# Optimization experiments

Hardware: AMD Instinct MI355X
Metric: run time of the kernel (lower is better)

The kernel has to match this reference:

```python
import jax, jax.numpy as jnp
import numpy as np

B, N, T = 16, 512, 12
IN, HID, HH, EMB, K, OUT = 2, 32, 32, 16, 2, 12


def setup_inputs() -> dict:
    key = jax.random.key(0)
    ks = jax.random.split(key, 32)
    def r(i, sh, s=1.0):
        return jax.random.normal(ks[i], sh, dtype=jnp.float32) * s
    return {
        "times": jnp.arange(T, dtype=jnp.float32),
        "coeff_a": r(0, (B, N, T - 1, IN)),
        "coeff_b": r(1, (B, N, T - 1, IN), 0.1),
        "coeff_c2": r(2, (B, N, T - 1, IN), 0.05),
        "coeff_d3": r(3, (B, N, T - 1, IN), 0.02),
        "Wh": r(4, (IN, HID), 0.3), "bh": r(5, (HID,), 0.01),
        "Wz": r(6, (IN, HID), 0.3), "bz": r(7, (HID,), 0.01),
        "fWin": r(8, (HID, HH), 0.15), "fbin": r(9, (HH,), 0.01),
        "fWmid": r(10, (HH, HH), 0.15), "fbmid": r(11, (HH,), 0.01),
        "fWout": r(12, (HH, HID * IN), 0.15), "fbout": r(13, (HID * IN,), 0.01),
        "gWin": r(14, (HID, HH), 0.15), "gbin": r(15, (HH,), 0.01),
        "gE": r(16, (N, EMB), 0.3),
        "gWpool": r(17, (EMB, K, HH, HH), 0.1),
        "gbpool": r(18, (EMB, HH), 0.1),
        "gWout": r(19, (HH, HID * HID), 0.05), "gbout": r(20, (HID * HID,), 0.01),
        "convW": r(21, (OUT, HID), 0.1), "convb": r(22, (OUT,), 0.01),
    }


def _forward(times, coeff_a, coeff_b, coeff_c2, coeff_d3, Wh, bh, Wz, bz,
             fWin, fbin, fWmid, fbmid, fWout, fbout,
             gWin, gbin, gE, gWpool, gbpool, gWout, gbout, convW, convb):
    maxlen = coeff_b.shape[2] - 1  # T - 2

    def dXdt(t):
        # NaturalCubicSpline.derivative: b + (two_c + three_d * frac) * frac
        idx = jnp.clip(jnp.sum(t > times) - 1, 0, maxlen)
        frac = t - times[idx]
        b = jnp.take(coeff_b, idx, axis=2)    # (B,N,IN)
        c2 = jnp.take(coeff_c2, idx, axis=2)
        d3 = jnp.take(coeff_d3, idx, axis=2)
        return b + (c2 + d3 * frac) * frac

    # adaptive graph conv supports + per-node weights (depend on params only)
    A = jax.nn.softmax(jax.nn.relu(gE @ gE.T), axis=1)   # (N,N)
    sup = [jnp.eye(N, dtype=A.dtype), A]
    for _ in range(2, K):
        sup.append(2.0 * A @ sup[-1] - sup[-2])
    supports = jnp.stack(sup, axis=0)                     # (K,N,N)
    aw = jnp.einsum('nd,dkio->nkio', gE, gWpool)          # (N,K,HH,HH)
    ab = gE @ gbpool                                      # (N,HH)

    def func_f(h):  # (B,N,HID) -> (B,N,HID,IN)
        x = jax.nn.relu(h @ fWin + fbin)
        x = jax.nn.relu(x @ fWmid + fbmid)
        return jnp.tanh((x @ fWout + fbout).reshape(*x.shape[:-1], HID, IN))

    def func_g(z):  # (B,N,HID) -> (B,N,HID,HID)
        x = jax.nn.relu(z @ gWin + gbin)                  # (B,N,HH)
        xg = jnp.einsum('knm,bmc->bnkc', supports, x)     # (B,N,K,HH)
        x = jnp.einsum('bnki,nkio->bno', xg, aw) + ab     # (B,N,HH)
        return jnp.tanh((x @ gWout + gbout).reshape(*x.shape[:-1], HID, HID))

    def vfield(t, h, z):
        dX = dXdt(t)                                      # (B,N,IN)
        vf = func_f(h)                                    # (B,N,HID,IN)
        vg = func_g(z)                                    # (B,N,HID,HID)
        fg = jnp.einsum('bnho,bnoi->bnhi', vg, vf)        # g(z) @ f(h)
        dh = jnp.einsum('bnhi,bni->bnh', vf, dX)
        dz = jnp.einsum('bnhi,bni->bnh', fg, dX)
        return dh, dz

    x0 = coeff_a[:, :, 0, :]          # spline.evaluate(times[0]) = a[...,0,:]
    h0 = x0 @ Wh + bh
    z0 = x0 @ Wz + bz

    def step(carry, tt):
        # torchdiffeq 'rk4' = RK4 with 3/8 rule (rk4_alt_step_func)
        h, z = carry
        t0, t1 = tt
        dt = t1 - t0
        third = dt / 3.0
        k1h, k1z = vfield(t0, h, z)
        k2h, k2z = vfield(t0 + third, h + third * k1h, z + third * k1z)
        k3h, k3z = vfield(t0 + 2.0 * third,
                          h + dt * (k2h - k1h / 3.0), z + dt * (k2z - k1z / 3.0))
        k4h, k4z = vfield(t1,
                          h + dt * (k1h - k2h + k3h), z + dt * (k1z - k2z + k3z))
        h = h + dt * 0.125 * (k1h + 3.0 * (k2h + k3h) + k4h)
        z = z + dt * 0.125 * (k1z + 3.0 * (k2z + k3z) + k4z)
        return (h, z), None

    (hT, zT), _ = jax.lax.scan(step, (h0, z0), (times[:-1], times[1:]))

    # end_conv: Conv2d(1, OUT, kernel=(1, HID)) on z_T (B,1,N,HID) -> (B,OUT,N,1)
    out = jnp.einsum('bnh,oh->bon', zT, convW) + convb[None, :, None]
    out = out.reshape(B, 1, OUT, N).transpose(0, 1, 3, 2)  # (B,1,N,OUT)
    return out


def reference(times, coeff_a, coeff_b, coeff_c2, coeff_d3, Wh, bh, Wz, bz,
              fWin, fbin, fWmid, fbmid, fWout, fbout,
              gWin, gbin, gE, gWpool, gbpool, gWout, gbout, convW, convb):
    return _forward(times, coeff_a, coeff_b, coeff_c2, coeff_d3, Wh, bh, Wz, bz,
                    fWin, fbin, fWmid, fbmid, fWout, fbout,
                    gWin, gbin, gE, gWpool, gbpool, gWout, gbout, convW, convb)
```

## Files before the change

### kernel.cpp

```cpp
#include <hip/hip_runtime.h>
#include <math.h>

#define NPTS 8192
#define NPS  (NPTS*32)

typedef __attribute__((ext_vector_type(8))) short bf16x8;
typedef __attribute__((ext_vector_type(4))) float f32x4;

__device__ __forceinline__ float tanh_fast(float x) {
  float e = __expf(2.0f*x);
  return 1.0f - 2.0f*__builtin_amdgcn_rcpf(e + 1.0f);
}
__device__ __forceinline__ unsigned short bf16h(float x) {
  unsigned u = __float_as_uint(x);
  return (unsigned short)((u + 0x7FFFu + ((u>>16)&1u)) >> 16);
}
__device__ __forceinline__ float bf16f(unsigned short h) {
  return __uint_as_float(((unsigned)h)<<16);
}
__device__ __forceinline__ bf16x8 pack_hi(const float* base) {
  bf16x8 H;
  #pragma unroll
  for (int jj = 0; jj < 4; ++jj) {
    float2 q = *(const float2*)(base + 2*jj);
// ... 76 lines not shown

__global__ void kPackGW(const float* __restrict__ gWout, short* __restrict__ GpkH,
                        short* __restrict__ GpkL) {
  int idx = blockIdx.x*256 + threadIdx.x;
  int j = idx & 7, l = (idx>>3)&63, tl = idx>>9;
  int col = tl*16 + (l&15);
  int k = ((l>>4)&3)*8 + j;
  float v = gWout[k*1024 + col];
  unsigned short hb = bf16h(v);
  GpkH[idx] = (short)hb;
  GpkL[idx] = (short)bf16h(v - bf16f(hb));
}

__global__ void kPackW(const float* __restrict__ fWin, const float* __restrict__ fWmid,
                       const float* __restrict__ fWout, const float* __restrict__ gWin,
                       short* __restrict__ WpkH, short* __restrict__ WpkL) {
  int idx = blockIdx.x*256 + threadIdx.x;
  if (idx >= 5120) return;
  int j = idx & 7, l = (idx>>3)&63, T = idx>>9;
  int k = ((l>>4)&3)*8 + j;
  const float* M; int cols, tl;
  if (T < 2)      { M = fWin;  cols = 32; tl = T;   }
  else if (T < 4) { M = fWmid; cols = 32; tl = T-2; }
  else if (T < 8) { M = fWout; cols = 64; tl = T-4; }
  else            { M = gWin;  cols = 32; tl = T-8; }
  float v = M[k*cols + tl*16 + (l&15)];
  unsigned short hb = bf16h(v);
  WpkH[idx] = (short)hb;
  WpkL[idx] = (short)bf16h(v - bf16f(hb));
}

__global__ void kDX(const float* __restrict__ cb, const float* __restrict__ cc2,
                    const float* __restrict__ cd3, float* __restrict__ dX) {
  int idx = blockIdx.x*256 + threadIdx.x;
  int slot = idx >> 14;
  int rem = idx & 16383;
  int p = rem >> 1, i = rem & 1;
  float v;
  if (slot == 0) {
    v = cb[p*22 + i];
  } else {
    int s1 = slot - 1;
    int k = s1 / 3, j = s1 - 3*k;
    float frac = (float)(j+1) * (1.0f/3.0f);
    if (j == 2) frac = 1.0f;
    int base = p*22 + k*2 + i;
    v = cb[base] + (cc2[base] + cd3[base]*frac)*frac;
  }
  dX[idx] = v;
}

__global__ void kInit(const float* __restrict__ ca, const float* __restrict__ Wh,
                      const float* __restrict__ bh, const float* __restrict__ Wz,
                      const float* __restrict__ bz, float* __restrict__ h,
                      float* __restrict__ z) {
  int idx = blockIdx.x*256 + threadIdx.x;
  int c = idx & 31, p = idx >> 5;
  float x0 = ca[p*22 + 0], x1 = ca[p*22 + 1];
  h[idx] = fmaf(x0, Wh[c], fmaf(x1, Wh[32+c], bh[c]));
  z[idx] = fmaf(x0, Wz[c], fmaf(x1, Wz[32+c], bz[c]));
}

__global__ void kXrel0(const float* __restrict__ z, const float* __restrict__ gWin,
                       const float* __restrict__ gbin, float* __restrict__ xrel,
                       short* __restrict__ xpkH) {
  __shared__ float zl[8][32];
  int t = threadIdx.x, pl = t >> 5, o = t & 31;
  int p = blockIdx.x*8 + pl;
  zl[pl][o] = z[p*32 + o];
  __syncthreads();
  float s = gbin[o];
  #pragma unroll
  for (int i = 0; i < 32; ++i) s = fmaf(zl[pl][i], gWin[i*32 + o], s);
  float xr = fmaxf(s, 0.f);
  xrel[p*32 + o] = xr;
  int b = p >> 9, m = p & 511;
  int c = m >> 5, rr = m & 31;
  int lane = (rr>>3)*16 + (o&15);
  int tt = o >> 4;
  size_t off = (((size_t)(b*16 + c)*2 + tt)*64 + lane)*8 + (rr&7);
  xpkH[off] = (short)bf16h(xr);
}

__global__ __launch_bounds__(512, 4) void kBF(
    const unsigned* __restrict__ awb, const float* __restrict__ ab,
    const float* __restrict__ dX, float* __restrict__ h, float* __restrict__ z,
    float* __restrict__ kh, float* __restrict__ kz,
    float* __restrict__ xrel,
    const short* __restrict__ ApkH, const short* __restrict__ ApkL,
    const short* __restrict__ xpkH, short* __restrict__ xpkHo,
    const short* __restrict__ GpkH, const short* __restrict__ GpkL,
    const short* __restrict__ WpkH, const short* __restrict__ WpkL,
    const float* __restrict__ fbin, const float* __restrict__ fbmid,
    const float* __restrict__ fbout, const float* __restrict__ gbin,
    const float* __restrict__ gbout, int stage, int slot)
{
  __shared__ float scrA[8][16][32];
  __shared__ float bGl[1024];
  __shared__ float HS[16*34], X1[16*34], X2[16*34], PLb[16*34];
  __shared__ float XR[16*36], AG[16*36];
  __shared__ float DHT[32*20];
  __shared__ float DZ[16*33];

  int t = threadIdx.x;
  int pl = t >> 5, o = t & 31;
  int w = t >> 6, l = t & 63;
  int ll = l & 15, lg = l >> 4;
  int bid = blockIdx.x;
  int xcd = bid & 7, sub = (bid >> 3) & 3, b = bid >> 5;
  int ntile = xcd*4 + sub;
  int pgbase = b*512 + ntile*16;
  int pg = pgbase + pl;

  bf16x8 gHreg[8];
  #pragma unroll
  for (int u = 0; u < 8; ++u)
    gHreg[u] = *(const bf16x8*)(GpkH + ((size_t)(w*8 + u)*64 + l)*8);

  bGl[t] = gbout[t]; bGl[t+512] = gbout[t+512];
  XR[pl*36 + o] = xrel[pg*32 + o];
  {
    float hv = h[pg*32 + o]; float hsv;
    if (stage == 1)      hsv = hv;
    else if (stage == 2) hsv = fmaf(kh[pg*32+o], (1.f/3.f), hv);
    else if (stage == 3) hsv = hv - (1.f/3.f)*kh[pg*32+o] + kh[NPS + pg*32+o];
    else                 hsv = hv + kh[pg*32+o] - kh[NPS + pg*32+o] + kh[2*NPS + pg*32+o];
    HS[pl*34 + o] = hsv;
  }

  {
    f32x4 acc0 = {0.f,0.f,0.f,0.f}, acc1 = {0.f,0.f,0.f,0.f};
    #pragma unroll
    for (int cc = 0; cc < 2; ++cc) {
      int c = w*2 + cc;
      size_t aoff = ((size_t)(ntile*16 + c)*64 + l)*8;
      bf16x8 aH = *(const bf16x8*)(ApkH + aoff);
      bf16x8 aL = *(const bf16x8*)(ApkL + aoff);
      size_t boff0 = (((size_t)(b*16 + c)*2 + 0)*64 + l)*8;
      size_t boff1 = (((size_t)(b*16 + c)*2 + 1)*64 + l)*8;
      bf16x8 bH0 = *(const bf16x8*)(xpkH + boff0);
      bf16x8 bH1 = *(const bf16x8*)(xpkH + boff1);
      acc0 = __builtin_amdgcn_mfma_f32_16x16x32_bf16(aL, bH0, acc0, 0, 0, 0);
      acc0 = __builtin_amdgcn_mfma_f32_16x16x32_bf16(aH, bH0, acc0, 0, 0, 0);
      acc1 = __builtin_amdgcn_mfma_f32_16x16x32_bf16(aL, bH1, acc1, 0, 0, 0);
      acc1 = __builtin_amdgcn_mfma_f32_16x16x32_bf16(aH, bH1, acc1, 0, 0, 0);
    }
    #pragma unroll
    for (int r = 0; r < 4; ++r) {
      scrA[w][lg*4+r][ll]      = acc0[r];
      scrA[w][lg*4+r][16 + ll] = acc1[r];
    }
  }
  __syncthreads();

  float plp0 = 0.f, plp1 = 0.f;
  if (w < 2) {
    bf16x8 aH = pack_hi(&HS[ll*34 + lg*8]);
    bf16x8 bH = *(const bf16x8*)(WpkH + (size_t)w*512 + l*8);
    bf16x8 bL = *(const bf16x8*)(WpkL + (size_t)w*512 + l*8);
    f32x4 acc = {0.f,0.f,0.f,0.f};
    acc = __builtin_amdgcn_mfma_f32_16x16x32_bf16(aH, bL, acc, 0, 0, 0);
    acc = __builtin_amdgcn_mfma_f32_16x16x32_bf16(aH, bH, acc, 0, 0, 0);
    int col = w*16 + ll;
    float bb = fbin[col];
    #pragma unroll
    for (int r = 0; r < 4; ++r) X1[(lg*4+r)*34 + col] = fmaxf(acc[r] + bb, 0.f);
  } else if (w < 4) {
    int base = (t - 128)*4;
    #pragma unroll
    for (int jj = 0; jj < 4; ++jj) {
      int s = base + jj; int sp = s>>5, so = s&31;
      float v = 0.f;
      #pragma unroll
      for (int ww = 0; ww < 8; ++ww) v += scrA[ww][sp][so];
      AG[sp*36 + so] = v;
    }
  } else {
    #pragma unroll
    for (int half = 0; half < 2; ++half) {
      int s = (t - 256) + half*256;
      int sp = s>>5, so = s&31;
      int nn = ntile*16 + sp;
      const unsigned* awp = awb + (size_t)nn*1024 + so;
      const float2* xr2 = (const float2*)&XR[sp*36];
      float acc = 0.f;
      #pragma unroll
      for (int q = 0; q < 16; ++q) {
        unsigned u = awp[q*32];
        float2 xv = xr2[q];
        acc = fmaf(xv.x, __uint_as_float(u << 16), acc);
        acc = fmaf(xv.y, __uint_as_float(u & 0xffff0000u), acc);
      }
      if (half == 0) plp0 = acc; else plp1 = acc;
    }
  }
  __syncthreads();

  if (w < 2) {
    bf16x8 aH = pack_hi(&X1[ll*34 + lg*8]);
    bf16x8 bH = *(const bf16x8*)(WpkH + (size_t)(2+w)*512 + l*8);
    bf16x8 bL = *(const bf16x8*)(WpkL + (size_t)(2+w)*512 + l*8);
    f32x4 acc = {0.f,0.f,0.f,0.f};
    acc = __builtin_amdgcn_mfma_f32_16x16x32_bf16(aH, bL, acc, 0, 0, 0);
    acc = __builtin_amdgcn_mfma_f32_16x16x32_bf16(aH, bH, acc, 0, 0, 0);
    int col = w*16 + ll;
    float bb = fbmid[col];
    #pragma unroll
    for (int r = 0; r < 4; ++r) X2[(lg*4+r)*34 + col] = fmaxf(acc[r] + bb, 0.f);
  } else if (w >= 4) {
    #pragma unroll
    for (int half = 0; half < 2; ++half) {
      int s = (t - 256) + half*256;
      int sp = s>>5, so = s&31;
      int nn = ntile*16 + sp;
      const unsigned* awp = awb + (size_t)nn*1024 + 512 + so;
      const float2* ag2 = (const float2*)&AG[sp*36];
      float acc = (half == 0) ? plp0 : plp1;
      #pragma unroll
      for (int q = 0; q < 16; ++q) {
        unsigned u = awp[q*32];
        float2 av = ag2[q];
        acc = fmaf(av.x, __uint_as_float(u << 16), acc);
        acc = fmaf(av.y, __uint_as_float(u & 0xffff0000u), acc);
      }
      PLb[sp*34 + so] = acc + ab[nn*32 + so];
    }
  }
  __syncthreads();

  if (w < 2) {
    bf16x8 aH = pack_hi(&X2[ll*34 + lg*8]);
    float vf[2][4];
    #pragma unroll
    for (int e = 0; e < 2; ++e) {
      int T = 2*w + e;
      bf16x8 bH = *(const bf16x8*)(WpkH + (size_t)(4+T)*512 + l*8);
      bf16x8 bL = *(const bf16x8*)(WpkL + (size_t)(4+T)*512 + l*8);
      f32x4 acc = {0.f,0.f,0.f,0.f};
      acc = __builtin_amdgcn_mfma_f32_16x16x32_bf16(aH, bL, acc, 0, 0, 0);
      acc = __builtin_amdgcn_mfma_f32_16x16x32_bf16(aH, bH, acc, 0, 0, 0);
      int col = T*16 + ll;
      float bb = fbout[col];
      #pragma unroll
      for (int r = 0; r < 4; ++r) vf[e][r] = tanh_fast(acc[r] + bb);
    }
    float2 dxv[4];
    #pragma unroll
    for (int r = 0; r < 4; ++r)
      dxv[r] = *(const float2*)&dX[(size_t)slot*16384 + (size_t)(pgbase + lg*4 + r)*2];
    #pragma unroll
    for (int e = 0; e < 2; ++e) {
      int T = 2*w + e;
      float vo[4];
      #pragma unroll
      for (int r = 0; r < 4; ++r) vo[r] = __shfl_xor(vf[e][r], 1);
      if (!(l & 1)) {
        int hh = T*8 + (ll>>1);
        float4 dv;
        dv.x = vf[e][0]*dxv[0].x + vo[0]*dxv[0].y;
        dv.y = vf[e][1]*dxv[1].x + vo[1]*dxv[1].y;
        dv.z = vf[e][2]*dxv[2].x + vo[2]*dxv[2].y;
        dv.w = vf[e][3]*dxv[3].x + vo[3]*dxv[3].y;
        *(float4*)&DHT[hh*20 + lg*4] = dv;
      }
    }
  }
  __syncthreads();

  {
    bf16x8 paH = pack_hi(&PLb[ll*34 + lg*8]);
    bf16x8 gLreg[8];
    #pragma unroll
    for (int u = 0; u < 8; ++u)
      gLreg[u] = *(const bf16x8*)(GpkL + ((size_t)(w*8 + u)*64 + l)*8);
    float p[4][4] = {{0.f,0.f,0.f,0.f},{0.f,0.f,0.f,0.f},{0.f,0.f,0.f,0.f},{0.f,0.f,0.f,0.f}};
    #pragma unroll
    for (int u = 0; u < 8; ++u) {
      f32x4 acc = {0.f,0.f,0.f,0.f};
      acc = __builtin_amdgcn_mfma_f32_16x16x32_bf16(paH, gLreg[u], acc, 0, 0, 0);
      acc = __builtin_amdgcn_mfma_f32_16x16x32_bf16(paH, gHreg[u], acc, 0, 0, 0);
      int tile = w*8 + u;
      int col = tile*16 + ll, oo = col & 31;
      float gb = bGl[col];
      float4 dh4 = *(const float4*)&DHT[oo*20 + lg*4];
      int h2 = u >> 1;
      float da[4] = {dh4.x, dh4.y, dh4.z, dh4.w};
      #pragma unroll
      for (int r = 0; r < 4; ++r) {
        float tv = tanh_fast(acc[r] + gb);
        p[r][h2] = fmaf(tv, da[r], p[r][h2]);
      }
    }
    #pragma unroll
    for (int r = 0; r < 4; ++r) {
      #pragma unroll
      for (int h2 = 0; h2 < 4; ++h2) {
        float v = p[r][h2];
        v += __shfl_xor(v, 1);
        v += __shfl_xor(v, 2);
        v += __shfl_xor(v, 4);
        v += __shfl_xor(v, 8);
        if (ll == r*4 + h2) DZ[(lg*4 + r)*33 + w*4 + h2] = v;
      }
    }
  }
  __syncthreads();

  {
    float dzv = DZ[pl*33 + o];
    float dhv = DHT[o*20 + pl];
    if (stage < 4) {
      kh[(size_t)(stage-1)*NPS + pg*32 + o] = dhv;
    } else {
      float hv = h[pg*32+o];
      float k1 = kh[pg*32+o], k2 = kh[NPS+pg*32+o], k3 = kh[2*NPS+pg*32+o];
      h[pg*32+o] = hv + 0.125f*(k1 + 3.f*(k2 + k3) + dhv);
    }
    float zv = z[pg*32 + o];
    float znv;
    if (stage == 1) {
      kz[pg*32+o] = dzv;
      znv = fmaf(dzv, (1.f/3.f), zv);
    } else if (stage == 2) {
      kz[NPS + pg*32+o] = dzv;
      znv = zv - (1.f/3.f)*kz[pg*32+o] + dzv;
    } else if (stage == 3) {
      kz[2*NPS + pg*32+o] = dzv;
      znv = zv + kz[pg*32+o] - kz[NPS+pg*32+o] + dzv;
    } else {
      float k1 = kz[pg*32+o], k2 = kz[NPS+pg*32+o], k3 = kz[2*NPS+pg*32+o];
      znv = zv + 0.125f*(k1 + 3.f*(k2 + k3) + dzv);
      z[pg*32+o] = znv;
    }
    X1[pl*34 + o] = znv;
  }
  __syncthreads();

  if (w < 2) {
    bf16x8 aH = pack_hi(&X1[ll*34 + lg*8]);
    bf16x8 bH = *(const bf16x8*)(WpkH + (size_t)(8+w)*512 + l*8);
    bf16x8 bL = *(const bf16x8*)(WpkL + (size_t)(8+w)*512 + l*8);
    f32x4 acc = {0.f,0.f,0.f,0.f};
    acc = __builtin_amdgcn_mfma_f32_16x16x32_bf16(aH, bL, acc, 0, 0, 0);
    acc = __builtin_amdgcn_mfma_f32_16x16x32_bf16(aH, bH, acc, 0, 0, 0);
    int col = w*16 + ll;
    float bb = gbin[col];
    int hp = ntile & 1, cch = ntile >> 1;
    #pragma unroll
    for (int r = 0; r < 4; ++r) {
      float xr = fmaxf(acc[r] + bb, 0.f);
      int row = lg*4 + r;
      xrel[(size_t)(pgbase + row)*32 + col] = xr;
      int rr = hp*16 + row;
      size_t off = (((size_t)(b*16 + cch)*2 + w)*64 + ((rr>>3)*16 + ll))*8 + (rr&7);
      xpkHo[off] = (short)bf16h(xr);
    }
  }
}

__global__ void kOut(const float* __restrict__ z, const float* __restrict__ convW,
                     const float* __restrict__ convb, float* __restrict__ out) {
  int idx = blockIdx.x*256 + threadIdx.x;
  int o = idx % 12, p = idx / 12;
  float s = convb[o];
  #pragma unroll
  for (int hh = 0; hh < 32; ++hh) s = fmaf(z[p*32 + hh], convW[o*32 + hh], s);
  out[idx] = s;
}

extern "C" void kernel_launch(void* const* d_in, const int* in_sizes, int n_in,
                              void* d_out, int out_size, void* d_ws, size_t ws_size,
                              hipStream_t stream) {
  (void)in_sizes; (void)n_in; (void)out_size; (void)ws_size;
  const float* ca     = (const float*)d_in[1];
  const float* cb     = (const float*)d_in[2];
  const float* cc2    = (const float*)d_in[3];
  const float* cd3    = (const float*)d_in[4];
  const float* Wh     = (const float*)d_in[5];
  const float* bh     = (const float*)d_in[6];
  const float* Wz     = (const float*)d_in[7];
  const float* bz     = (const float*)d_in[8];
  const float* fWin   = (const float*)d_in[9];
  const float* fbin   = (const float*)d_in[10];
  const float* fWmid  = (const float*)d_in[11];
  const float* fbmid  = (const float*)d_in[12];
  const float* fWout  = (const float*)d_in[13];
  const float* fbout  = (const float*)d_in[14];
  const float* gWin   = (const float*)d_in[15];
  const float* gbin   = (const float*)d_in[16];
  const float* gE     = (const float*)d_in[17];
  const float* gWpool = (const float*)d_in[18];
  const float* gbpool = (const float*)d_in[19];
  const float* gWout  = (const float*)d_in[20];
  const float* gbout  = (const float*)d_in[21];
  const float* convW  = (const float*)d_in[22];
  const float* convb  = (const float*)d_in[23];
  float* out = (float*)d_out;

  float* wsf  = (float*)d_ws;
  unsigned* awb = (unsigned*)wsf;
  float* wAb  = wsf + 524288;
  float* wDX  = wAb + 16384;
  float* wH   = wDX + 557056;
  float* wZ   = wH + 262144;
  float* wKh  = wZ + 262144;
  float* wKz  = wKh + 786432;
  float* wXr  = wKz + 786432;
  short* ApkH = (short*)(wXr + 262144);
  short* ApkL = ApkH + 262144;
  short* xp0H = ApkL + 262144;
  short* xp1H = xp0H + 262144;
  short* GpkH = xp1H + 262144;
  short* GpkL = GpkH + 32768;
  short* WpkH = GpkL + 32768;
  short* WpkL = WpkH + 5120;

  kA_softmax<<<512, 256, 0, stream>>>(gE, ApkH, ApkL);
  kAwB<<<512, 256, 0, stream>>>(gE, gWpool, gbpool, awb, wAb);
  kPackGW<<<128, 256, 0, stream>>>(gWout, GpkH, GpkL);
  kPackW<<<20, 256, 0, stream>>>(fWin, fWmid, fWout, gWin, WpkH, WpkL);
  kDX<<<2176, 256, 0, stream>>>(cb, cc2, cd3, wDX);
  kInit<<<1024, 256, 0, stream>>>(ca, Wh, bh, Wz, bz, wH, wZ);
  kXrel0<<<1024, 256, 0, stream>>>(wZ, gWin, gbin, wXr, xp0H);

  for (int ss = 0; ss < 44; ++ss) {
    int stage = (ss & 3) + 1;
    int step = ss >> 2;
    int slot = (ss == 0) ? 0 : (3*step + (ss & 3));
    const short* xiH = (ss & 1) ? xp1H : xp0H;
    short* xoH = (ss & 1) ? xp0H : xp1H;
    kBF<<<512, 512, 0, stream>>>(awb, wAb, wDX, wH, wZ, wKh, wKz, wXr,
                                 ApkH, ApkL, xiH, xoH, GpkH, GpkL,
                                 WpkH, WpkL, fbin, fbmid, fbout, gbin, gbout,
                                 stage, slot);
  }
  kOut<<<384, 256, 0, stream>>>(wZ, convW, convb, out);
}
```

Baseline: 689.6 us.

## Fuse 44 RK stage launches into one persistent kernel with per-batch barriers

Replaces the 44 separate kBF launches with a single persistent kernel that loops over all RK stages. Blocks in the same batch synchronise through an atomic counter barrier. Node-local state (h, z, k stages, xrel, MLP weights, biases, graph-conv A operands) stays in LDS and registers across stages instead of round-tripping through global memory. This removes launch overhead and global traffic but needs all 512 blocks co-resident to avoid deadlock, and the spin barrier has a timeout guard that could silently break correctness.

```diff
diff --git a/kernel.cpp b/kernel.cpp
--- a/kernel.cpp
+++ b/kernel.cpp
@@ -182,18 +182,35 @@
   xpkH[off] = (short)bf16h(xr);
 }
 
-__global__ __launch_bounds__(512, 4) void kBF(
+
+__device__ __forceinline__ void batch_barrier(unsigned* __restrict__ cnt, unsigned target) {
+  __syncthreads();
+  if (threadIdx.x == 0) {
+    __threadfence();
+    __hip_atomic_fetch_add(cnt, 1u, __ATOMIC_RELEASE, __HIP_MEMORY_SCOPE_AGENT);
+    unsigned v = __hip_atomic_load(cnt, __ATOMIC_ACQUIRE, __HIP_MEMORY_SCOPE_AGENT);
+    unsigned guard = 0;
+    while (v < target) {
+      if (++guard > (1u<<20)) break;
+      __builtin_amdgcn_s_sleep(8);
+      v = __hip_atomic_load(cnt, __ATOMIC_ACQUIRE, __HIP_MEMORY_SCOPE_AGENT);
+    }
+    __threadfence();
+  }
+  __syncthreads();
+}
+
+__global__ __launch_bounds__(512, 4) void kPersist(
     const unsigned* __restrict__ awb, const float* __restrict__ ab,
-    const float* __restrict__ dX, float* __restrict__ h, float* __restrict__ z,
-    float* __restrict__ kh, float* __restrict__ kz,
-    float* __restrict__ xrel,
+    const float* __restrict__ dX, const float* __restrict__ h0,
+    float* __restrict__ zio, const float* __restrict__ xrel0,
+    short* __restrict__ xp0H, short* __restrict__ xp1H,
     const short* __restrict__ ApkH, const short* __restrict__ ApkL,
-    const short* __restrict__ xpkH, short* __restrict__ xpkHo,
     const short* __restrict__ GpkH, const short* __restrict__ GpkL,
     const short* __restrict__ WpkH, const short* __restrict__ WpkL,
     const float* __restrict__ fbin, const float* __restrict__ fbmid,
     const float* __restrict__ fbout, const float* __restrict__ gbin,
-    const float* __restrict__ gbout, int stage, int slot)
+    const float* __restrict__ gbout, unsigned* __restrict__ bar)
 {
   __shared__ float scrA[8][16][32];
   __shared__ float bGl[1024];
@@ -201,6 +218,10 @@
   __shared__ float XR[16*36], AG[16*36];
   __shared__ float DHT[32*20];
   __shared__ float DZ[16*33];
+  __shared__ short WH_l[5120], WL_l[5120];
+  __shared__ float bF[160];
+  __shared__ float abS[512];
+  __shared__ float hS[512], zS[512], khS[3*512], kzS[3*512];
 
   int t = threadIdx.x;
   int pl = t >> 5, o = t & 31;
@@ -210,252 +231,275 @@
   int xcd = bid & 7, sub = (bid >> 3) & 3, b = bid >> 5;
   int ntile = xcd*4 + sub;
   int pgbase = b*512 + ntile*16;
-  int pg = pgbase + pl;
-
+  unsigned* cnt = bar + b*64;
+
+  bGl[t] = gbout[t]; bGl[t+512] = gbout[t+512];
+  for (int j = t; j < 5120; j += 512) { WH_l[j] = WpkH[j]; WL_l[j] = WpkL[j]; }
+  if (t < 32) bF[t] = fbin[t];
+  else if (t < 64) bF[t] = fbmid[t-32];
+  else if (t < 128) bF[t] = fbout[t-64];
+  else if (t < 160) bF[t] = gbin[t-128];
+  abS[t] = ab[(size_t)(ntile*16 + pl)*32 + o];
   bf16x8 gHreg[8];
   #pragma unroll
   for (int u = 0; u < 8; ++u)
     gHreg[u] = *(const bf16x8*)(GpkH + ((size_t)(w*8 + u)*64 + l)*8);
-
-  bGl[t] = gbout[t]; bGl[t+512] = gbout[t+512];
-  XR[pl*36 + o] = xrel[pg*32 + o];
-  {
-    float hv = h[pg*32 + o]; float hsv;
-    if (stage == 1)      hsv = hv;
-    else if (stage == 2) hsv = fmaf(kh[pg*32+o], (1.f/3.f), hv);
-    else if (stage == 3) hsv = hv - (1.f/3.f)*kh[pg*32+o] + kh[NPS + pg*32+o];
-    else                 hsv = hv + kh[pg*32+o] - kh[NPS + pg*32+o] + kh[2*NPS + pg*32+o];
-    HS[pl*34 + o] = hsv;
-  }
-
-  {
-    f32x4 acc0 = {0.f,0.f,0.f,0.f}, acc1 = {0.f,0.f,0.f,0.f};
-    #pragma unroll
-    for (int cc = 0; cc < 2; ++cc) {
-      int c = w*2 + cc;
-      size_t aoff = ((size_t)(ntile*16 + c)*64 + l)*8;
-      bf16x8 aH = *(const bf16x8*)(ApkH + aoff);
-      bf16x8 aL = *(const bf16x8*)(ApkL + aoff);
-      size_t boff0 = (((size_t)(b*16 + c)*2 + 0)*64 + l)*8;
-      size_t boff1 = (((size_t)(b*16 + c)*2 + 1)*64 + l)*8;
-      bf16x8 bH0 = *(const bf16x8*)(xpkH + boff0);
-      bf16x8 bH1 = *(const bf16x8*)(xpkH + boff1);
-      acc0 = __builtin_amdgcn_mfma_f32_16x16x32_bf16(aL, bH0, acc0, 0, 0, 0);
-      acc0 = __builtin_amdgcn_mfma_f32_16x16x32_bf16(aH, bH0, acc0, 0, 0, 0);
-      acc1 = __builtin_amdgcn_mfma_f32_16x16x32_bf16(aL, bH1, acc1, 0, 0, 0);
-      acc1 = __builtin_amdgcn_mfma_f32_16x16x32_bf16(aH, bH1, acc1, 0, 0, 0);
-    }
-    #pragma unroll
-    for (int r = 0; r < 4; ++r) {
-      scrA[w][lg*4+r][ll]      = acc0[r];
-      scrA[w][lg*4+r][16 + ll] = acc1[r];
-    }
-  }
-  __syncthreads();
-
-  float plp0 = 0.f, plp1 = 0.f;
-  if (w < 2) {
-    bf16x8 aH = pack_hi(&HS[ll*34 + lg*8]);
-    bf16x8 bH = *(const bf16x8*)(WpkH + (size_t)w*512 + l*8);
-    bf16x8 bL = *(const bf16x8*)(WpkL + (size_t)w*512 + l*8);
-    f32x4 acc = {0.f,0.f,0.f,0.f};
-    acc = __builtin_amdgcn_mfma_f32_16x16x32_bf16(aH, bL, acc, 0, 0, 0);
-    acc = __builtin_amdgcn_mfma_f32_16x16x32_bf16(aH, bH, acc, 0, 0, 0);
-    int col = w*16 + ll;
-    float bb = fbin[col];
-    #pragma unroll
-    for (int r = 0; r < 4; ++r) X1[(lg*4+r)*34 + col] = fmaxf(acc[r] + bb, 0.f);
-  } else if (w < 4) {
-    int base = (t - 128)*4;
-    #pragma unroll
-    for (int jj = 0; jj < 4; ++jj) {
-      int s = base + jj; int sp = s>>5, so = s&31;
-      float v = 0.f;
-      #pragma unroll
-      for (int ww = 0; ww < 8; ++ww) v += scrA[ww][sp][so];
-      AG[sp*36 + so] = v;
-    }
-  } else {
-    #pragma unroll
-    for (int half = 0; half < 2; ++half) {
-      int s = (t - 256) + half*256;
-      int sp = s>>5, so = s&31;
-      int nn = ntile*16 + sp;
-      const unsigned* awp = awb + (size_t)nn*1024 + so;
-      const float2* xr2 = (const float2*)&XR[sp*36];
-      float acc = 0.f;
-      #pragma unroll
-      for (int q = 0; q < 16; ++q) {
-        unsigned u = awp[q*32];
-        float2 xv = xr2[q];
-        acc = fmaf(xv.x, __uint_as_float(u << 16), acc);
-        acc = fmaf(xv.y, __uint_as_float(u & 0xffff0000u), acc);
-      }
-      if (half == 0) plp0 = acc; else plp1 = acc;
-    }
-  }
-  __syncthreads();
-
-  if (w < 2) {
-    bf16x8 aH = pack_hi(&X1[ll*34 + lg*8]);
-    bf16x8 bH = *(const bf16x8*)(WpkH + (size_t)(2+w)*512 + l*8);
-    bf16x8 bL = *(const bf16x8*)(WpkL + (size_t)(2+w)*512 + l*8);
-    f32x4 acc = {0.f,0.f,0.f,0.f};
-    acc = __builtin_amdgcn_mfma_f32_16x16x32_bf16(aH, bL, acc, 0, 0, 0);
-    acc = __builtin_amdgcn_mfma_f32_16x16x32_bf16(aH, bH, acc, 0, 0, 0);
-    int col = w*16 + ll;
-    float bb = fbmid[col];
-    #pragma unroll
-    for (int r = 0; r < 4; ++r) X2[(lg*4+r)*34 + col] = fmaxf(acc[r] + bb, 0.f);
-  } else if (w >= 4) {
-    #pragma unroll
-    for (int half = 0; half < 2; ++half) {
-      int s = (t - 256) + half*256;
-      int sp = s>>5, so = s&31;
-      int nn = ntile*16 + sp;
-      const unsigned* awp = awb + (size_t)nn*1024 + 512 + so;
-      const float2* ag2 = (const float2*)&AG[sp*36];
-      float acc = (half == 0) ? plp0 : plp1;
-      #pragma unroll
-      for (int q = 0; q < 16; ++q) {
-        unsigned u = awp[q*32];
-        float2 av = ag2[q];
-        acc = fmaf(av.x, __uint_as_float(u << 16), acc);
-        acc = fmaf(av.y, __uint_as_float(u & 0xffff0000u), acc);
-      }
-      PLb[sp*34 + so] = acc + ab[nn*32 + so];
-    }
-  }
-  __syncthreads();
-
-  if (w < 2) {
-    bf16x8 aH = pack_hi(&X2[ll*34 + lg*8]);
-    float vf[2][4];
-    #pragma unroll
-    for (int e = 0; e < 2; ++e) {
-      int T = 2*w + e;
-      bf16x8 bH = *(const bf16x8*)(WpkH + (size_t)(4+T)*512 + l*8);
-      bf16x8 bL = *(const bf16x8*)(WpkL + (size_t)(4+T)*512 + l*8);
+  bf16x8 aH2[2], aL2[2];
+  #pragma unroll
+  for (int cc = 0; cc < 2; ++cc) {
+    size_t aoff = ((size_t)(ntile*16 + w*2 + cc)*64 + l)*8;
+    aH2[cc] = *(const bf16x8*)(ApkH + aoff);
+    aL2[cc] = *(const bf16x8*)(ApkL + aoff);
+  }
+  hS[t] = h0[(size_t)pgbase*32 + t];
+  zS[t] = zio[(size_t)pgbase*32 + t];
+  XR[pl*36 + o] = xrel0[(size_t)(pgbase + pl)*32 + o];
+  __syncthreads();
+
+  #pragma unroll 1
+  for (int ss = 0; ss < 44; ++ss) {
+    int stage = (ss & 3) + 1;
+    int step = ss >> 2;
+    int slot = (ss == 0) ? 0 : (3*step + (ss & 3));
+    const short* xiH = (ss & 1) ? xp1H : xp0H;
+    short* xoH = (ss & 1) ? xp0H : xp1H;
+
+    {
+      float hv = hS[t]; float hsv;
+      if (stage == 1)      hsv = hv;
+      else if (stage == 2) hsv = fmaf(khS[t], (1.f/3.f), hv);
+      else if (stage == 3) hsv = hv - (1.f/3.f)*khS[t] + khS[512 + t];
+      else                 hsv = hv + khS[t] - khS[512 + t] + khS[1024 + t];
+      HS[pl*34 + o] = hsv;
+    }
+
+    {
+      f32x4 acc0 = {0.f,0.f,0.f,0.f}, acc1 = {0.f,0.f,0.f,0.f};
+      #pragma unroll
+      for (int cc = 0; cc < 2; ++cc) {
+        int c = w*2 + cc;
+        size_t boff0 = (((size_t)(b*16 + c)*2 + 0)*64 + l)*8;
+        bf16x8 bH0 = *(const bf16x8*)(xiH + boff0);
+        bf16x8 bH1 = *(const bf16x8*)(xiH + boff0 + 512);
+        acc0 = __builtin_amdgcn_mfma_f32_16x16x32_bf16(aL2[cc], bH0, acc0, 0, 0, 0);
+        acc0 = __builtin_amdgcn_mfma_f32_16x16x32_bf16(aH2[cc], bH0, acc0, 0, 0, 0);
+        acc1 = __builtin_amdgcn_mfma_f32_16x16x32_bf16(aL2[cc], bH1, acc1, 0, 0, 0);
+        acc1 = __builtin_amdgcn_mfma_f32_16x16x32_bf16(aH2[cc], bH1, acc1, 0, 0, 0);
+      }
+      #pragma unroll
+      for (int r = 0; r < 4; ++r) {
+        scrA[w][lg*4+r][ll]      = acc0[r];
+        scrA[w][lg*4+r][16 + ll] = acc1[r];
+      }
+    }
+    __syncthreads();
+
+    float plp0 = 0.f, plp1 = 0.f;
+    if (w < 2) {
+      bf16x8 aH = pack_hi(&HS[ll*34 + lg*8]);
+      bf16x8 bH = *(const bf16x8*)(WH_l + w*512 + l*8);
+      bf16x8 bL = *(const bf16x8*)(WL_l + w*512 + l*8);
       f32x4 acc = {0.f,0.f,0.f,0.f};
       acc = __builtin_amdgcn_mfma_f32_16x16x32_bf16(aH, bL, acc, 0, 0, 0);
       acc = __builtin_amdgcn_mfma_f32_16x16x32_bf16(aH, bH, acc, 0, 0, 0);
-      int col = T*16 + ll;
-      float bb = fbout[col];
-      #pragma unroll
-      for (int r = 0; r < 4; ++r) vf[e][r] = tanh_fast(acc[r] + bb);
-    }
-    float2 dxv[4];
-    #pragma unroll
-    for (int r = 0; r < 4; ++r)
-      dxv[r] = *(const float2*)&dX[(size_t)slot*16384 + (size_t)(pgbase + lg*4 + r)*2];
-    #pragma unroll
-    for (int e = 0; e < 2; ++e) {
-      int T = 2*w + e;
-      float vo[4];
-      #pragma unroll
-      for (int r = 0; r < 4; ++r) vo[r] = __shfl_xor(vf[e][r], 1);
-      if (!(l & 1)) {
-        int hh = T*8 + (ll>>1);
-        float4 dv;
-        dv.x = vf[e][0]*dxv[0].x + vo[0]*dxv[0].y;
-        dv.y = vf[e][1]*dxv[1].x + vo[1]*dxv[1].y;
-        dv.z = vf[e][2]*dxv[2].x + vo[2]*dxv[2].y;
-        dv.w = vf[e][3]*dxv[3].x + vo[3]*dxv[3].y;
-        *(float4*)&DHT[hh*20 + lg*4] = dv;
-      }
-    }
-  }
-  __syncthreads();
-
-  {
-    bf16x8 paH = pack_hi(&PLb[ll*34 + lg*8]);
-    bf16x8 gLreg[8];
-    #pragma unroll
-    for (int u = 0; u < 8; ++u)
-      gLreg[u] = *(const bf16x8*)(GpkL + ((size_t)(w*8 + u)*64 + l)*8);
-    float p[4][4] = {{0.f,0.f,0.f,0.f},{0.f,0.f,0.f,0.f},{0.f,0.f,0.f,0.f},{0.f,0.f,0.f,0.f}};
-    #pragma unroll
-    for (int u = 0; u < 8; ++u) {
+      int col = w*16 + ll;
+      float bb = bF[col];
+      #pragma unroll
+      for (int r = 0; r < 4; ++r) X1[(lg*4+r)*34 + col] = fmaxf(acc[r] + bb, 0.f);
+    } else if (w < 4) {
+      int base = (t - 128)*4;
+      #pragma unroll
+      for (int jj = 0; jj < 4; ++jj) {
+        int s = base + jj; int sp = s>>5, so = s&31;
+        float v = 0.f;
+        #pragma unroll
+        for (int ww = 0; ww < 8; ++ww) v += scrA[ww][sp][so];
+        AG[sp*36 + so] = v;
+      }
+    } else {
+      #pragma unroll
+      for (int half = 0; half < 2; ++half) {
+        int s = (t - 256) + half*256;
+        int sp = s>>5, so = s&31;
+        int nn = ntile*16 + sp;
+        const unsigned* awp = awb + (size_t)nn*1024 + so;
+        const float2* xr2 = (const float2*)&XR[sp*36];
+        float acc = 0.f;
+        #pragma unroll
+        for (int q = 0; q < 16; ++q) {
+          unsigned u = awp[q*32];
+          float2 xv = xr2[q];
+          acc = fmaf(xv.x, __uint_as_float(u << 16), acc);
+          acc = fmaf(xv.y, __uint_as_float(u & 0xffff0000u), acc);
+        }
+        if (half == 0) plp0 = acc; else plp1 = acc;
+      }
+    }
+    __syncthreads();
+
+    if (w < 2) {
+      bf16x8 aH = pack_hi(&X1[ll*34 + lg*8]);
+      bf16x8 bH = *(const bf16x8*)(WH_l + (2+w)*512 + l*8);
+      bf16x8 bL = *(const bf16x8*)(WL_l + (2+w)*512 + l*8);
       f32x4 acc = {0.f,0.f,0.f,0.f};
-      acc = __builtin_amdgcn_mfma_f32_16x16x32_bf16(paH, gLreg[u], acc, 0, 0, 0);
-      acc = __builtin_amdgcn_mfma_f32_16x16x32_bf16(paH, gHreg[u], acc, 0, 0, 0);
-      int tile = w*8 + u;
-      int col = tile*16 + ll, oo = col & 31;
-      float gb = bGl[col];
-      float4 dh4 = *(const float4*)&DHT[oo*20 + lg*4];
-      int h2 = u >> 1;
-      float da[4] = {dh4.x, dh4.y, dh4.z, dh4.w};
+      acc = __builtin_amdgcn_mfma_f32_16x16x32_bf16(aH, bL, acc, 0, 0, 0);
+      acc = __builtin_amdgcn_mfma_f32_16x16x32_bf16(aH, bH, acc, 0, 0, 0);
+      int col = w*16 + ll;
+      float bb = bF[32 + col];
+      #pragma unroll
+      for (int r = 0; r < 4; ++r) X2[(lg*4+r)*34 + col] = fmaxf(acc[r] + bb, 0.f);
+    } else if (w >= 4) {
+      #pragma unroll
+      for (int half = 0; half < 2; ++half) {
+        int s = (t - 256) + half*256;
+        int sp = s>>5, so = s&31;
+        int nn = ntile*16 + sp;
+        const unsigned* awp = awb + (size_t)nn*1024 + 512 + so;
+        const float2* ag2 = (const float2*)&AG[sp*36];
+        float acc = (half == 0) ? plp0 : plp1;
+        #pragma unroll
+        for (int q = 0; q < 16; ++q) {
+          unsigned u = awp[q*32];
+          float2 av = ag2[q];
+          acc = fmaf(av.x, __uint_as_float(u << 16), acc);
+          acc = fmaf(av.y, __uint_as_float(u & 0xffff0000u), acc);
+        }
+        PLb[sp*34 + so] = acc + abS[s];
+      }
+    }
+    __syncthreads();
+
+    if (w < 2) {
+      bf16x8 aH = pack_hi(&X2[ll*34 + lg*8]);
+      float vf[2][4];
+      #pragma unroll
+      for (int e = 0; e < 2; ++e) {
+        int T = 2*w + e;
+        bf16x8 bH = *(const bf16x8*)(WH_l + (4+T)*512 + l*8);
+        bf16x8 bL = *(const bf16x8*)(WL_l + (4+T)*512 + l*8);
+        f32x4 acc = {0.f,0.f,0.f,0.f};
+        acc = __builtin_amdgcn_mfma_f32_16x16x32_bf16(aH, bL, acc, 0, 0, 0);
+        acc = __builtin_amdgcn_mfma_f32_16x16x32_bf16(aH, bH, acc, 0, 0, 0);
+        int col = T*16 + ll;
+        float bb = bF[64 + col];
+        #pragma unroll
+        for (int r = 0; r < 4; ++r) vf[e][r] = tanh_fast(acc[r] + bb);
+      }
+      float2 dxv[4];
+      #pragma unroll
+      for (int r = 0; r < 4; ++r)
+        dxv[r] = *(const float2*)&dX[(size_t)slot*16384 + (size_t)(pgbase + lg*4 + r)*2];
+      #pragma unroll
+      for (int e = 0; e < 2; ++e) {
+        int T = 2*w + e;
+        float vo[4];
+        #pragma unroll
+        for (int r = 0; r < 4; ++r) vo[r] = __shfl_xor(vf[e][r], 1);
+        if (!(l & 1)) {
+          int hh = T*8 + (ll>>1);
+          float4 dv;
+          dv.x = vf[e][0]*dxv[0].x + vo[0]*dxv[0].y;
+          dv.y = vf[e][1]*dxv[1].x + vo[1]*dxv[1].y;
+          dv.z = vf[e][2]*dxv[2].x + vo[2]*dxv[2].y;
+          dv.w = vf[e][3]*dxv[3].x + vo[3]*dxv[3].y;
+          *(float4*)&DHT[hh*20 + lg*4] = dv;
+        }
+      }
+    }
+    __syncthreads();
+
+    {
+      bf16x8 paH = pack_hi(&PLb[ll*34 + lg*8]);
+      bf16x8 gLreg[8];
+      #pragma unroll
+      for (int u = 0; u < 8; ++u)
+        gLreg[u] = *(const bf16x8*)(GpkL + ((size_t)(w*8 + u)*64 + l)*8);
+      float p[4][4] = {{0.f,0.f,0.f,0.f},{0.f,0.f,0.f,0.f},{0.f,0.f,0.f,0.f},{0.f,0.f,0.f,0.f}};
+      #pragma unroll
+      for (int u = 0; u < 8; ++u) {
+        f32x4 acc = {0.f,0.f,0.f,0.f};
+        acc = __builtin_amdgcn_mfma_f32_16x16x32_bf16(paH, gLreg[u], acc, 0, 0, 0);
+        acc = __builtin_amdgcn_mfma_f32_16x16x32_bf16(paH, gHreg[u], acc, 0, 0, 0);
+        int tile = w*8 + u;
+        int col = tile*16 + ll, oo = col & 31;
+        float gb = bGl[col];
+        float4 dh4 = *(const float4*)&DHT[oo*20 + lg*4];
+        int h2 = u >> 1;
+        float da[4] = {dh4.x, dh4.y, dh4.z, dh4.w};
+        #pragma unroll
+        for (int r = 0; r < 4; ++r) {
+          float tv = tanh_fast(acc[r] + gb);
+          p[r][h2] = fmaf(tv, da[r], p[r][h2]);
+        }
+      }
       #pragma unroll
       for (int r = 0; r < 4; ++r) {
-        float tv = tanh_fast(acc[r] + gb);
-        p[r][h2] = fmaf(tv, da[r], p[r][h2]);
-      }
-    }
-    #pragma unroll
-    for (int r = 0; r < 4; ++r) {
-      #pragma unroll
-      for (int h2 = 0; h2 < 4; ++h2) {
-        float v = p[r][h2];
-        v += __shfl_xor(v, 1);
-        v += __shfl_xor(v, 2);
-        v += __shfl_xor(v, 4);
-        v += __shfl_xor(v, 8);
-        if (ll == r*4 + h2) DZ[(lg*4 + r)*33 + w*4 + h2] = v;
-      }
-    }
-  }
-  __syncthreads();
-
-  {
-    float dzv = DZ[pl*33 + o];
-    float dhv = DHT[o*20 + pl];
-    if (stage < 4) {
-      kh[(size_t)(stage-1)*NPS + pg*32 + o] = dhv;
-    } else {
-      float hv = h[pg*32+o];
-      float k1 = kh[pg*32+o], k2 = kh[NPS+pg*32+o], k3 = kh[2*NPS+pg*32+o];
-      h[pg*32+o] = hv + 0.125f*(k1 + 3.f*(k2 + k3) + dhv);
-    }
-    float zv = z[pg*32 + o];
-    float znv;
-    if (stage == 1) {
-      kz[pg*32+o] = dzv;
-      znv = fmaf(dzv, (1.f/3.f), zv);
-    } else if (stage == 2) {
-      kz[NPS + pg*32+o] = dzv;
-      znv = zv - (1.f/3.f)*kz[pg*32+o] + dzv;
-    } else if (stage == 3) {
-      kz[2*NPS + pg*32+o] = dzv;
-      znv = zv + kz[pg*32+o] - kz[NPS+pg*32+o] + dzv;
-    } else {
-      float k1 = kz[pg*32+o], k2 = kz[NPS+pg*32+o], k3 = kz[2*NPS+pg*32+o];
-      znv = zv + 0.125f*(k1 + 3.f*(k2 + k3) + dzv);
-      z[pg*32+o] = znv;
-    }
-    X1[pl*34 + o] = znv;
-  }
-  __syncthreads();
-
-  if (w < 2) {
-    bf16x8 aH = pack_hi(&X1[ll*34 + lg*8]);
-    bf16x8 bH = *(const bf16x8*)(WpkH + (size_t)(8+w)*512 + l*8);
-    bf16x8 bL = *(const bf16x8*)(WpkL + (size_t)(8+w)*512 + l*8);
-    f32x4 acc = {0.f,0.f,0.f,0.f};
-    acc = __builtin_amdgcn_mfma_f32_16x16x32_bf16(aH, bL, acc, 0, 0, 0);
-    acc = __builtin_amdgcn_mfma_f32_16x16x32_bf16(aH, bH, acc, 0, 0, 0);
-    int col = w*16 + ll;
-    float bb = gbin[col];
-    int hp = ntile & 1, cch = ntile >> 1;
-    #pragma unroll
-    for (int r = 0; r < 4; ++r) {
-      float xr = fmaxf(acc[r] + bb, 0.f);
-      int row = lg*4 + r;
-      xrel[(size_t)(pgbase + row)*32 + col] = xr;
-      int rr = hp*16 + row;
-      size_t off = (((size_t)(b*16 + cch)*2 + w)*64 + ((rr>>3)*16 + ll))*8 + (rr&7);
-      xpkHo[off] = (short)bf16h(xr);
-    }
-  }
+        #pragma unroll
+        for (int h2 = 0; h2 < 4; ++h2) {
+          float v = p[r][h2];
+          v += __shfl_xor(v, 1);
+          v += __shfl_xor(v, 2);
+          v += __shfl_xor(v, 4);
+          v += __shfl_xor(v, 8);
+          if (ll == r*4 + h2) DZ[(lg*4 + r)*33 + w*4 + h2] = v;
+        }
+      }
+    }
+    __syncthreads();
+
+    {
+      float dzv = DZ[pl*33 + o];
+      float dhv = DHT[o*20 + pl];
+      if (stage < 4) {
+        khS[(stage-1)*512 + t] = dhv;
+      } else {
+        float k1 = khS[t], k2 = khS[512+t], k3 = khS[1024+t];
+        hS[t] = hS[t] + 0.125f*(k1 + 3.f*(k2 + k3) + dhv);
+      }
+      float zv = zS[t], znv;
+      if (stage == 1) {
+        kzS[t] = dzv;
+        znv = fmaf(dzv, (1.f/3.f), zv);
+      } else if (stage == 2) {
+        kzS[512 + t] = dzv;
+        znv = zv - (1.f/3.f)*kzS[t] + dzv;
+      } else if (stage == 3) {
+        kzS[1024 + t] = dzv;
+        znv = zv + kzS[t] - kzS[512+t] + dzv;
+      } else {
+        float k1 = kzS[t], k2 = kzS[512+t], k3 = kzS[1024+t];
+        znv = zv + 0.125f*(k1 + 3.f*(k2 + k3) + dzv);
+        zS[t] = znv;
+      }
+      X1[pl*34 + o] = znv;
+    }
+    __syncthreads();
+
+    if (w < 2) {
+      bf16x8 aH = pack_hi(&X1[ll*34 + lg*8]);
+      bf16x8 bH = *(const bf16x8*)(WH_l + (8+w)*512 + l*8);
+      bf16x8 bL = *(const bf16x8*)(WL_l + (8+w)*512 + l*8);
+      f32x4 acc = {0.f,0.f,0.f,0.f};
+      acc = __builtin_amdgcn_mfma_f32_16x16x32_bf16(aH, bL, acc, 0, 0, 0);
+      acc = __builtin_amdgcn_mfma_f32_16x16x32_bf16(aH, bH, acc, 0, 0, 0);
+      int col = w*16 + ll;
+      float bb = bF[128 + col];
+      int hp = ntile & 1, cch = ntile >> 1;
+      #pragma unroll
+      for (int r = 0; r < 4; ++r) {
+        float xr = fmaxf(acc[r] + bb, 0.f);
+        int row = lg*4 + r;
+        XR[row*36 + col] = xr;
+        int rr = hp*16 + row;
+        size_t off = (((size_t)(b*16 + cch)*2 + w)*64 + ((rr>>3)*16 + ll))*8 + (rr&7);
+        xoH[off] = (short)bf16h(xr);
+      }
+    }
+
+    if (ss < 43) batch_barrier(cnt, 32u*(ss+1));
+  }
+
+  zio[(size_t)pgbase*32 + t] = zS[t];
 }
 
 __global__ void kOut(const float* __restrict__ z, const float* __restrict__ convW,
@@ -503,9 +547,7 @@
   float* wDX  = wAb + 16384;
   float* wH   = wDX + 557056;
   float* wZ   = wH + 262144;
-  float* wKh  = wZ + 262144;
-  float* wKz  = wKh + 786432;
-  float* wXr  = wKz + 786432;
+  float* wXr  = wZ + 262144;
   short* ApkH = (short*)(wXr + 262144);
   short* ApkL = ApkH + 262144;
   short* xp0H = ApkL + 262144;
@@ -514,7 +556,9 @@
   short* GpkL = GpkH + 32768;
   short* WpkH = GpkL + 32768;
   short* WpkL = WpkH + 5120;
-
+  unsigned* bar = (unsigned*)(WpkL + 5120);
+
+  hipMemsetAsync(bar, 0, 1024*sizeof(unsigned), stream);
   kA_softmax<<<512, 256, 0, stream>>>(gE, ApkH, ApkL);
   kAwB<<<512, 256, 0, stream>>>(gE, gWpool, gbpool, awb, wAb);
   kPackGW<<<128, 256, 0, stream>>>(gWout, GpkH, GpkL);
@@ -523,16 +567,10 @@
   kInit<<<1024, 256, 0, stream>>>(ca, Wh, bh, Wz, bz, wH, wZ);
   kXrel0<<<1024, 256, 0, stream>>>(wZ, gWin, gbin, wXr, xp0H);
 
-  for (int ss = 0; ss < 44; ++ss) {
-    int stage = (ss & 3) + 1;
-    int step = ss >> 2;
-    int slot = (ss == 0) ? 0 : (3*step + (ss & 3));
-    const short* xiH = (ss & 1) ? xp1H : xp0H;
-    short* xoH = (ss & 1) ? xp0H : xp1H;
-    kBF<<<512, 512, 0, stream>>>(awb, wAb, wDX, wH, wZ, wKh, wKz, wXr,
-                                 ApkH, ApkL, xiH, xoH, GpkH, GpkL,
-                                 WpkH, WpkL, fbin, fbmid, fbout, gbin, gbout,
-                                 stage, slot);
-  }
+  kPersist<<<512, 512, 0, stream>>>(awb, wAb, wDX, wH, wZ, wXr,
+                                    xp0H, xp1H, ApkH, ApkL, GpkH, GpkL,
+                                    WpkH, WpkL, fbin, fbmid, fbout, gbin, gbout,
+                                    bar);
+
   kOut<<<384, 256, 0, stream>>>(wZ, convW, convb, out);
 }
```

Measured after the change: 2.724 ms. 295% more time.

## Merge barrier-separated MLP and graph-pool phases into one synchronized block

Applied to the files above, without the earlier changes.

Warps 0 and 1 now run the whole three-layer MLP chain (input, mid, output) back to back. Each computes both 16-column tiles of X1 and X2 itself, so it only reads LDS it wrote. Warps 4 and up do the AG reduction and then both pooling dot-products in one pass over rows they own. This removes two __syncthreads per vector-field evaluation. The cost is duplicated MFMA work in warps 0 and 1, idle warps 2 and 3, and a longer critical path on the MLP warps.

```diff
diff --git a/kernel.cpp b/kernel.cpp
--- a/kernel.cpp
+++ b/kernel.cpp
@@ -237,9 +237,8 @@
       bf16x8 aH = *(const bf16x8*)(ApkH + aoff);
       bf16x8 aL = *(const bf16x8*)(ApkL + aoff);
       size_t boff0 = (((size_t)(b*16 + c)*2 + 0)*64 + l)*8;
-      size_t boff1 = (((size_t)(b*16 + c)*2 + 1)*64 + l)*8;
       bf16x8 bH0 = *(const bf16x8*)(xpkH + boff0);
-      bf16x8 bH1 = *(const bf16x8*)(xpkH + boff1);
+      bf16x8 bH1 = *(const bf16x8*)(xpkH + boff0 + 512);
       acc0 = __builtin_amdgcn_mfma_f32_16x16x32_bf16(aL, bH0, acc0, 0, 0, 0);
       acc0 = __builtin_amdgcn_mfma_f32_16x16x32_bf16(aH, bH0, acc0, 0, 0, 0);
       acc1 = __builtin_amdgcn_mfma_f32_16x16x32_bf16(aL, bH1, acc1, 0, 0, 0);
@@ -253,29 +252,84 @@
   }
   __syncthreads();
 
-  float plp0 = 0.f, plp1 = 0.f;
   if (w < 2) {
-    bf16x8 aH = pack_hi(&HS[ll*34 + lg*8]);
-    bf16x8 bH = *(const bf16x8*)(WpkH + (size_t)w*512 + l*8);
-    bf16x8 bL = *(const bf16x8*)(WpkL + (size_t)w*512 + l*8);
-    f32x4 acc = {0.f,0.f,0.f,0.f};
-    acc = __builtin_amdgcn_mfma_f32_16x16x32_bf16(aH, bL, acc, 0, 0, 0);
-    acc = __builtin_amdgcn_mfma_f32_16x16x32_bf16(aH, bH, acc, 0, 0, 0);
-    int col = w*16 + ll;
-    float bb = fbin[col];
-    #pragma unroll
-    for (int r = 0; r < 4; ++r) X1[(lg*4+r)*34 + col] = fmaxf(acc[r] + bb, 0.f);
-  } else if (w < 4) {
-    int base = (t - 128)*4;
-    #pragma unroll
-    for (int jj = 0; jj < 4; ++jj) {
-      int s = base + jj; int sp = s>>5, so = s&31;
+    {
+      bf16x8 aH = pack_hi(&HS[ll*34 + lg*8]);
+      #pragma unroll
+      for (int tile = 0; tile < 2; ++tile) {
+        bf16x8 bH = *(const bf16x8*)(WpkH + (size_t)tile*512 + l*8);
+        bf16x8 bL = *(const bf16x8*)(WpkL + (size_t)tile*512 + l*8);
+        f32x4 acc = {0.f,0.f,0.f,0.f};
+        acc = __builtin_amdgcn_mfma_f32_16x16x32_bf16(aH, bL, acc, 0, 0, 0);
+        acc = __builtin_amdgcn_mfma_f32_16x16x32_bf16(aH, bH, acc, 0, 0, 0);
+        int col = tile*16 + ll;
+        float bb = fbin[col];
+        #pragma unroll
+        for (int r = 0; r < 4; ++r) X1[(lg*4+r)*34 + col] = fmaxf(acc[r] + bb, 0.f);
+      }
+    }
+    {
+      bf16x8 aH = pack_hi(&X1[ll*34 + lg*8]);
+      #pragma unroll
+      for (int tile = 0; tile < 2; ++tile) {
+        bf16x8 bH = *(const bf16x8*)(WpkH + (size_t)(2+tile)*512 + l*8);
+        bf16x8 bL = *(const bf16x8*)(WpkL + (size_t)(2+tile)*512 + l*8);
+        f32x4 acc = {0.f,0.f,0.f,0.f};
+        acc = __builtin_amdgcn_mfma_f32_16x16x32_bf16(aH, bL, acc, 0, 0, 0);
+        acc = __builtin_amdgcn_mfma_f32_16x16x32_bf16(aH, bH, acc, 0, 0, 0);
+        int col = tile*16 + ll;
+        float bb = fbmid[col];
+        #pragma unroll
+        for (int r = 0; r < 4; ++r) X2[(lg*4+r)*34 + col] = fmaxf(acc[r] + bb, 0.f);
+      }
+    }
+    {
+      bf16x8 aH = pack_hi(&X2[ll*34 + lg*8]);
+      float vf[2][4];
+      #pragma unroll
+      for (int e = 0; e < 2; ++e) {
+        int T = 2*w + e;
+        bf16x8 bH = *(const bf16x8*)(WpkH + (size_t)(4+T)*512 + l*8);
+        bf16x8 bL = *(const bf16x8*)(WpkL + (size_t)(4+T)*512 + l*8);
+        f32x4 acc = {0.f,0.f,0.f,0.f};
+        acc = __builtin_amdgcn_mfma_f32_16x16x32_bf16(aH, bL, acc, 0, 0, 0);
+        acc = __builtin_amdgcn_mfma_f32_16x16x32_bf16(aH, bH, acc, 0, 0, 0);
+        int col = T*16 + ll;
+        float bb = fbout[col];
+        #pragma unroll
+        for (int r = 0; r < 4; ++r) vf[e][r] = tanh_fast(acc[r] + bb);
+      }
+      float2 dxv[4];
+      #pragma unroll
+      for (int r = 0; r < 4; ++r)
+        dxv[r] = *(const float2*)&dX[(size_t)slot*16384 + (size_t)(pgbase + lg*4 + r)*2];
+      #pragma unroll
+      for (int e = 0; e < 2; ++e) {
+        int T = 2*w + e;
+        float vo[4];
+        #pragma unroll
+        for (int r = 0; r < 4; ++r) vo[r] = __shfl_xor(vf[e][r], 1);
+        if (!(l & 1)) {
+          int hh = T*8 + (ll>>1);
+          float4 dv;
+          dv.x = vf[e][0]*dxv[0].x + vo[0]*dxv[0].y;
+          dv.y = vf[e][1]*dxv[1].x + vo[1]*dxv[1].y;
+          dv.z = vf[e][2]*dxv[2].x + vo[2]*dxv[2].y;
+          dv.w = vf[e][3]*dxv[3].x + vo[3]*dxv[3].y;
+          *(float4*)&DHT[hh*20 + lg*4] = dv;
+        }
+      }
+    }
+  } else if (w >= 4) {
+    #pragma unroll
+    for (int half = 0; half < 2; ++half) {
+      int s = (t - 256) + half*256;
+      int sp = s>>5, so = s&31;
       float v = 0.f;
       #pragma unroll
       for (int ww = 0; ww < 8; ++ww) v += scrA[ww][sp][so];
       AG[sp*36 + so] = v;
     }
-  } else {
     #pragma unroll
     for (int half = 0; half < 2; ++half) {
       int s = (t - 256) + half*256;
@@ -283,6 +337,7 @@
       int nn = ntile*16 + sp;
       const unsigned* awp = awb + (size_t)nn*1024 + so;
       const float2* xr2 = (const float2*)&XR[sp*36];
+      const float2* ag2 = (const float2*)&AG[sp*36];
       float acc = 0.f;
       #pragma unroll
       for (int q = 0; q < 16; ++q) {
@@ -291,78 +346,14 @@
         acc = fmaf(xv.x, __uint_as_float(u << 16), acc);
         acc = fmaf(xv.y, __uint_as_float(u & 0xffff0000u), acc);
       }
-      if (half == 0) plp0 = acc; else plp1 = acc;
-    }
-  }
-  __syncthreads();
-
-  if (w < 2) {
-    bf16x8 aH = pack_hi(&X1[ll*34 + lg*8]);
-    bf16x8 bH = *(const bf16x8*)(WpkH + (size_t)(2+w)*512 + l*8);
-    bf16x8 bL = *(const bf16x8*)(WpkL + (size_t)(2+w)*512 + l*8);
-    f32x4 acc = {0.f,0.f,0.f,0.f};
-    acc = __builtin_amdgcn_mfma_f32_16x16x32_bf16(aH, bL, acc, 0, 0, 0);
-    acc = __builtin_amdgcn_mfma_f32_16x16x32_bf16(aH, bH, acc, 0, 0, 0);
-    int col = w*16 + ll;
-    float bb = fbmid[col];
-    #pragma unroll
-    for (int r = 0; r < 4; ++r) X2[(lg*4+r)*34 + col] = fmaxf(acc[r] + bb, 0.f);
-  } else if (w >= 4) {
-    #pragma unroll
-    for (int half = 0; half < 2; ++half) {
-      int s = (t - 256) + half*256;
-      int sp = s>>5, so = s&31;
-      int nn = ntile*16 + sp;
-      const unsigned* awp = awb + (size_t)nn*1024 + 512 + so;
-      const float2* ag2 = (const float2*)&AG[sp*36];
-      float acc = (half == 0) ? plp0 : plp1;
       #pragma unroll
       for (int q = 0; q < 16; ++q) {
-        unsigned u = awp[q*32];
+        unsigned u = awp[512 + q*32];
         float2 av = ag2[q];
         acc = fmaf(av.x, __uint_as_float(u << 16), acc);
         acc = fmaf(av.y, __uint_as_float(u & 0xffff0000u), acc);
       }
       PLb[sp*34 + so] = acc + ab[nn*32 + so];
-    }
-  }
-  __syncthreads();
-
-  if (w < 2) {
-    bf16x8 aH = pack_hi(&X2[ll*34 + lg*8]);
-    float vf[2][4];
-    #pragma unroll
-    for (int e = 0; e < 2; ++e) {
-      int T = 2*w + e;
-      bf16x8 bH = *(const bf16x8*)(WpkH + (size_t)(4+T)*512 + l*8);
-      bf16x8 bL = *(const bf16x8*)(WpkL + (size_t)(4+T)*512 + l*8);
-      f32x4 acc = {0.f,0.f,0.f,0.f};
-      acc = __builtin_amdgcn_mfma_f32_16x16x32_bf16(aH, bL, acc, 0, 0, 0);
-      acc = __builtin_amdgcn_mfma_f32_16x16x32_bf16(aH, bH, acc, 0, 0, 0);
-      int col = T*16 + ll;
-      float bb = fbout[col];
-      #pragma unroll
-      for (int r = 0; r < 4; ++r) vf[e][r] = tanh_fast(acc[r] + bb);
-    }
-    float2 dxv[4];
-    #pragma unroll
-    for (int r = 0; r < 4; ++r)
-      dxv[r] = *(const float2*)&dX[(size_t)slot*16384 + (size_t)(pgbase + lg*4 + r)*2];
-    #pragma unroll
-    for (int e = 0; e < 2; ++e) {
-      int T = 2*w + e;
-      float vo[4];
-      #pragma unroll
-      for (int r = 0; r < 4; ++r) vo[r] = __shfl_xor(vf[e][r], 1);
-      if (!(l & 1)) {
-        int hh = T*8 + (ll>>1);
-        float4 dv;
-        dv.x = vf[e][0]*dxv[0].x + vo[0]*dxv[0].y;
-        dv.y = vf[e][1]*dxv[1].x + vo[1]*dxv[1].y;
-        dv.z = vf[e][2]*dxv[2].x + vo[2]*dxv[2].y;
-        dv.w = vf[e][3]*dxv[3].x + vo[3]*dxv[3].y;
-        *(float4*)&DHT[hh*20 + lg*4] = dv;
-      }
     }
   }
   __syncthreads();
```

After: 574.3 us. -16.7%, faster.
